# Performance work log

Measured on AMD Instinct MI355X. Metric: run time of the kernel, lower is better.

The kernel has to match this reference:

```python
import jax, jax.numpy as jnp
import numpy as np

EPS = 1e-8
LN_EPS = 1e-5
DIM, NHEADS = 512, 8
HEAD_DIM = DIM // NHEADS
SCALE = HEAD_DIM ** -0.5
ROLE_VOCAB = 8


def _layernorm(x, g, b):
    mu = x.mean(-1, keepdims=True)
    var = ((x - mu) ** 2).mean(-1, keepdims=True)
    return (x - mu) * jax.lax.rsqrt(var + LN_EPS) * g + b


def setup_inputs() -> dict:
    key = jax.random.key(0)
    ks = jax.random.split(key, 16)
    B, K, L, D = 8, 4, 1024, DIM
    s = 1.0 / np.sqrt(D)
    return {
        "state_repr": jax.random.normal(ks[0], (B, K, L, D), jnp.float32),
        "residue_mask": jax.random.randint(ks[1], (B, K, L), 0, 2) > 0,
        "state_weights": jax.random.uniform(ks[2], (B, K), jnp.float32),
        "state_roles": jax.random.randint(ks[3], (B, K), 0, ROLE_VOCAB),
        "state_present_mask": jnp.ones((B, K), dtype=bool),
        "role_emb": jax.random.normal(ks[4], (ROLE_VOCAB, D), jnp.float32),
        "Wq": jax.random.normal(ks[5], (D, D), jnp.float32) * s,
        "Wk": jax.random.normal(ks[6], (D, D), jnp.float32) * s,
        "Wv": jax.random.normal(ks[7], (D, D), jnp.float32) * s,
        "Wo": jax.random.normal(ks[8], (D, D), jnp.float32) * s,
        "ln1_g": jnp.ones((3 * D,), jnp.float32),
        "ln1_b": jnp.zeros((3 * D,), jnp.float32),
        "Wg1": jax.random.normal(ks[9], (D, 3 * D), jnp.float32) / np.sqrt(3 * D),
        "bg1": jnp.zeros((D,), jnp.float32),
        "Wg2": jax.random.normal(ks[10], (D, D), jnp.float32) * s,
        "bg2": jnp.zeros((D,), jnp.float32),
        "norm_g": jnp.ones((D,), jnp.float32),
        "norm_b": jnp.zeros((D,), jnp.float32),
    }


def _forward(state_repr, residue_mask, state_weights, state_roles, state_present_mask,
             role_emb, Wq, Wk, Wv, Wo, ln1_g, ln1_b, Wg1, bg1, Wg2, bg2, norm_g, norm_b):
    B, K, L, D = state_repr.shape
    H, hd = NHEADS, HEAD_DIM
    roles = jnp.maximum(state_roles, 0)
    role_e = role_emb[roles][:, :, None, :]                       # [B,K,1,D]
    valid = residue_mask & state_present_mask[:, :, None]          # [B,K,L]

    # normalized state weights
    pres = state_present_mask.astype(jnp.float32)
    w = state_weights.astype(jnp.float32) * pres
    denom = w.sum(1, keepdims=True)
    fallback = pres / jnp.maximum(pres.sum(1, keepdims=True), 1.0)
    nsw = jnp.where(denom > EPS, w / jnp.maximum(denom, EPS), fallback)  # [B,K]

    x = (state_repr + role_e) * valid[..., None]
    x = x.transpose(0, 2, 1, 3)                                    # [B,L,K,D]
    valid_rlk = valid.transpose(0, 2, 1)                           # [B,L,K]

    def proj(W):  # torch Linear: y = x @ W.T
        return (x @ W.T).reshape(B, L, K, H, hd).transpose(0, 1, 3, 2, 4)  # [B,L,H,K,hd]

    q, k, v = proj(Wq), proj(Wk), proj(Wv)
    logits = jnp.einsum('blhqd,blhkd->blhqk', q, k) * SCALE
    logits = logits + jnp.log(jnp.maximum(nsw, EPS))[:, None, None, None, :]
    key_mask = valid_rlk[:, :, None, None, :]                      # [B,L,1,1,K]
    logits = jnp.where(key_mask, logits, -jnp.inf)
    attn = jax.nn.softmax(logits, axis=-1)
    attn = jnp.nan_to_num(attn, nan=0.0, posinf=0.0, neginf=0.0)
    attn_out = jnp.einsum('blhqk,blhkd->blhqd', attn, v)
    attn_out = attn_out.transpose(0, 1, 3, 2, 4).reshape(B, L, K, D)
    attn_out = (attn_out @ Wo.T) * valid_rlk[..., None]

    swr = nsw[:, None, :] * valid_rlk.astype(jnp.float32)          # [B,L,K]
    swr = swr / jnp.maximum(swr.sum(-1, keepdims=True), EPS)
    weighted_mean = jnp.sum(x * swr[..., None], axis=2)            # [B,L,D]
    attn_pooled = jnp.sum(attn_out * swr[..., None], axis=2)

    max_in = jnp.where(valid_rlk[..., None], x, -1e9)
    max_feat = max_in.max(axis=2)
    has_any = valid_rlk.any(axis=2, keepdims=True)
    max_feat = jnp.where(has_any, max_feat, 0.0)

    fusion_base = 0.5 * (attn_pooled + weighted_mean)
    gate_in = jnp.concatenate([attn_pooled, weighted_mean, max_feat], axis=-1)
    h = _layernorm(gate_in, ln1_g, ln1_b)
    h = jax.nn.gelu(h @ Wg1.T + bg1, approximate=False)
    gate = jax.nn.sigmoid(h @ Wg2.T + bg2)
    fused = gate * fusion_base + (1.0 - gate) * max_feat
    fused = _layernorm(fused + weighted_mean, norm_g, norm_b)

    attn_mean = attn.mean(axis=(2, 3))                             # [B,L,K]
    return fused, attn_pooled, weighted_mean, max_feat, attn_mean, nsw


def reference(state_repr, residue_mask, state_weights, state_roles, state_present_mask,
              role_emb, Wq, Wk, Wv, Wo, ln1_g, ln1_b, Wg1, bg1, Wg2, bg2, norm_g, norm_b):
    return _forward(state_repr, residue_mask, state_weights, state_roles, state_present_mask,
                    role_emb, Wq, Wk, Wv, Wo, ln1_g, ln1_b, Wg1, bg1, Wg2, bg2, norm_g, norm_b)
```

## Files before the change

kernel.cpp:

```cpp
#include <hip/hip_runtime.h>
#include <math.h>

#define BB 8
#define KK 4
#define LL 1024
#define DD 512
#define HD 64
#define D3 1536
#define MM (BB*LL*KK)
#define BL (BB*LL)
#define SCALE 0.125f
#define EPSF 1e-8f
#define LN_EPSF 1e-5f

typedef _Float16 hfrag __attribute__((ext_vector_type(8)));
typedef float f32x4 __attribute__((ext_vector_type(4)));

__device__ __forceinline__ unsigned short f2h(float f) {
    _Float16 h = (_Float16)f;
    unsigned short u; __builtin_memcpy(&u, &h, 2); return u;
}
__device__ __forceinline__ float h2f(unsigned short u) {
    _Float16 h; __builtin_memcpy(&h, &u, 2); return (float)h;
}

__device__ __forceinline__ void glds16(const unsigned short* g, unsigned short* l) {
    __builtin_amdgcn_global_load_lds(
        (const __attribute__((address_space(1))) void*)g,
        (__attribute__((address_space(3))) void*)l, 16, 0, 0);
}

__device__ __forceinline__ void nsw_compute(const float* sw, const int* pres,
                                            int b, float* nswv) {
    float w[KK], pr[KK]; float denom = 0.f, ps = 0.f;
    #pragma unroll
    for (int k = 0; k < KK; ++k) {
        pr[k] = pres[b*KK + k] ? 1.f : 0.f;
        w[k]  = sw[b*KK + k] * pr[k];
        denom += w[k]; ps += pr[k];
    }
    #pragma unroll
    for (int k = 0; k < KK; ++k)
        nswv[k] = (denom > EPSF) ? w[k] / fmaxf(denom, EPSF)
                                 : pr[k] / fmaxf(ps, 1.f);
}

#define WSZ 262144
#define OG1 1048576
#define OG2 1835008
#define WTOT 2097152
__global__ __launch_bounds__(256) void cvt_weights(
        const float* __restrict__ Wq, const float* __restrict__ Wk,
        const float* __restrict__ Wv, const float* __restrict__ Wo,
        const float* __restrict__ Wg1, const float* __restrict__ Wg2,
        unsigned short* __restrict__ dst) {
    int t = blockIdx.x * 256 + threadIdx.x;
    int e = t * 4;
    const float* src; int off;
    if      (e < WSZ)    { src = Wq;  off = e; }
    else if (e < 2*WSZ)  { src = Wk;  off = e - WSZ; }
    else if (e < 3*WSZ)  { src = Wv;  off = e - 2*WSZ; }
    else if (e < OG1)    { src = Wo;  off = e - 3*WSZ; }
    else if (e < OG2)    { src = Wg1; off = e - OG1; }
    else                 { src = Wg2; off = e - OG2; }
    float4 v = *(const float4*)(src + off);
    ushort4 o;
    o.x = f2h(v.x); o.y = f2h(v.y); o.z = f2h(v.z); o.w = f2h(v.w);
    *(ushort4*)(dst + e) = o;
}

__global__ __launch_bounds__(256) void buildx_kernel(
        const float* __restrict__ SR, const int* __restrict__ residue,
        const int* __restrict__ pres, const int* __restrict__ roles,
        const float* __restrict__ role_emb, const float* __restrict__ sw,
        unsigned short* __restrict__ Xh, float* __restrict__ rowmask,
        float* __restrict__ out_wm, float* __restrict__ out_mx,
        float* __restrict__ f_nsw) {
    int t  = blockIdx.x * 256 + threadIdx.x;
    int bl = t >> 7;
    int d4 = (t & 127) << 2;
    int b  = bl >> 10, l = bl & 1023;
    float nswv[KK];
    nsw_compute(sw, pres, b, nswv);
    float mk[KK], swr[KK];
    float ssum = 0.f, many = 0.f;
    #pragma unroll
    for (int k = 0; k < KK; ++k) {
        int bk = b*KK + k;
        bool valid = (residue[(size_t)bk*LL + l] != 0) && (pres[bk] != 0);
        mk[k]  = valid ? 1.f : 0.f;
        swr[k] = nswv[k] * mk[k];
        ssum += swr[k]; many += mk[k];
    }
    float inv = 1.f / fmaxf(ssum, EPSF);
    bool hasany = many > 0.5f;
    float wmx = 0.f, wmy = 0.f, wmz = 0.f, wmw = 0.f;
    float mxx = -1e9f, mxy = -1e9f, mxz = -1e9f, mxw = -1e9f;
    #pragma unroll
    for (int k = 0; k < KK; ++k) {
        int bk = b*KK + k;
        int role = roles[bk]; if (role < 0) role = 0;
        float4 sr = *(const float4*)(SR + ((size_t)bk*LL + l)*DD + d4);
        float4 re = *(const float4*)(role_emb + (size_t)role*DD + d4);
        float xx = (sr.x + re.x)*mk[k], xy = (sr.y + re.y)*mk[k];
        float xz = (sr.z + re.z)*mk[k], xw = (sr.w + re.w)*mk[k];
        ushort4 xs; xs.x = f2h(xx); xs.y = f2h(xy); xs.z = f2h(xz); xs.w = f2h(xw);
        *(ushort4*)(Xh + (size_t)(bl*KK + k)*DD + d4) = xs;
        float s = swr[k]*inv;
        wmx = fmaf(xx, s, wmx); wmy = fmaf(xy, s, wmy);
        wmz = fmaf(xz, s, wmz); wmw = fmaf(xw, s, wmw);
        if (mk[k] > 0.5f) {
            mxx = fmaxf(mxx, xx); mxy = fmaxf(mxy, xy);
            mxz = fmaxf(mxz, xz); mxw = fmaxf(mxw, xw);
        }
    }
    if (!hasany) { mxx = mxy = mxz = mxw = 0.f; }
    float4 wmv; wmv.x = wmx; wmv.y = wmy; wmv.z = wmz; wmv.w = wmw;
    float4 mxv; mxv.x = mxx; mxv.y = mxy; mxv.z = mxz; mxv.w = mxw;
    *(float4*)(out_wm + (size_t)bl*DD + d4) = wmv;
    *(float4*)(out_mx + (size_t)bl*DD + d4) = mxv;
    if (d4 == 0) {
        #pragma unroll
        for (int k = 0; k < KK; ++k) rowmask[bl*KK + k] = mk[k];
    }
    if (blockIdx.x == 0 && threadIdx.x < BB*KK) {
        int bb = threadIdx.x >> 2, kk2 = threadIdx.x & 3;
        float nv[KK];
        nsw_compute(sw, pres, bb, nv);
        f_nsw[threadIdx.x] = nv[kk2];
    }
}

template<int TM, int EPI, int OUTH, int QKVR, int SWZ>
__global__ __launch_bounds__(256) void gemm_mfma(
        const unsigned short* __restrict__ A, const unsigned short* __restrict__ W,
        void* __restrict__ Cv, int M, int N, int Kd,
        const float* __restrict__ bias, const float* __restrict__ rowmask) {
    constexpr int FI = TM / 32;
    __shared__ __align__(16) unsigned short As[TM*32];
    __shared__ __align__(16) unsigned short Bs[128*32];
    const int tid  = threadIdx.x;
    const int wave = tid >> 6, lane = tid & 63;
    int m0, n0;
    if (SWZ) {
        int id = blockIdx.x;
        int c = id & 7, j = id >> 3;
        int mloc = j / 12;
        m0 = (c*32 + mloc) * TM;
        n0 = (j - mloc*12) * 128;
    } else {
        m0 = blockIdx.y * TM; n0 = blockIdx.x * 128;
    }
    const int srow = lane >> 2;
    const int scol = (lane & 3) << 3;
    const int arow = (TM == 128) ? (wave*32 + srow)
                   : (TM == 64)  ? (wave*16 + srow)
                   :               ((wave & 1)*16 + srow);
    const bool astage = (TM >= 64) || (wave < 2);
    const unsigned short* Ag0 = A + (size_t)(m0 + arow) * Kd + scol;
    const unsigned short* Ag1 = Ag0 + (size_t)16 * Kd;
    unsigned short* Al0 = As + arow*32 + scol;
    unsigned short* Al1 = Al0 + 16*32;
    const unsigned short* Wp0 = W + (size_t)(n0 + wave*32 + srow) * Kd + scol;
    const unsigned short* Wp1 = Wp0 + (size_t)16 * Kd;
    unsigned short* Bl0 = Bs + (wave*32 + srow)*32 + scol;
    unsigned short* Bl1 = Bl0 + 16*32;
    const int wr = (wave >> 1) * (TM/2);
    const int wc = (wave & 1) * 64;
    const int fr = lane & 15;
    const int fq = (lane >> 4) * 8;
    f32x4 acc[FI][4] = {};
    for (int k0 = 0; k0 < Kd; k0 += 32) {
        if (astage)    glds16(Ag0 + k0, Al0);
        if (TM == 128) glds16(Ag1 + k0, Al1);
        glds16(Wp0 + k0, Bl0);
        glds16(Wp1 + k0, Bl1);
        __syncthreads();
        hfrag af[FI], bf[4];
        #pragma unroll
        for (int i = 0; i < FI; ++i)
            af[i] = *(const hfrag*)(As + (wr + i*16 + fr)*32 + fq);
        #pragma unroll
        for (int j = 0; j < 4; ++j)
            bf[j] = *(const hfrag*)(Bs + (wc + j*16 + fr)*32 + fq);
        #pragma unroll
        for (int i = 0; i < FI; ++i)
            #pragma unroll
            for (int j = 0; j < 4; ++j)
                acc[i][j] = __builtin_amdgcn_mfma_f32_16x16x32_f16(af[i], bf[j], acc[i][j], 0, 0, 0);
        __syncthreads();
    }
    unsigned short* Ch = (unsigned short*)Cv;
    int Nout = N, colbase = n0;
    if (QKVR) {
        const int seg = n0 >> 9;
        Ch = (unsigned short*)Cv + (size_t)seg * M * 512;
        Nout = 512;
        colbase = n0 - (seg << 9);
    }
    #pragma unroll
    for (int i = 0; i < FI; ++i) {
        const int row = m0 + wr + i*16 + (lane >> 4)*4;
        #pragma unroll
        for (int j = 0; j < 4; ++j) {
            const int col = colbase + wc + j*16 + (lane & 15);
            float bv = (EPI == 2) ? bias[col] : 0.f;
            #pragma unroll
            for (int r = 0; r < 4; ++r) {
                float v = acc[i][j][r];
                if (EPI == 2) { v += bv; v = 0.5f * v * (1.f + erff(v * 0.70710678118654752f)); }
                if (OUTH) Ch[(size_t)(row + r) * Nout + col] = f2h(v);
                else      ((float*)Cv)[(size_t)(row + r) * Nout + col] = v;
            }
        }
    }
}

__global__ __launch_bounds__(256) void wo_pool_kernel(
        const unsigned short* __restrict__ A,
        const unsigned short* __restrict__ W,
        const float* __restrict__ sw, const int* __restrict__ pres,
        const float* __restrict__ rmask,
        const float* __restrict__ in_wm, const float* __restrict__ in_mx,
        const float* __restrict__ ln1_g, const float* __restrict__ ln1_b,
        float* __restrict__ out_ap, unsigned short* __restrict__ hin) {
    __shared__ __align__(16) unsigned short As[32*32];
    __shared__ __align__(16) unsigned short Bs[512*32];
    const int tid = threadIdx.x, wave = tid >> 6, lane = tid & 63;
    const int m0 = blockIdx.x * 32;
    const int srow = lane >> 2, scol = (lane & 3) << 3;
    const unsigned short* Ag = A + (size_t)(m0 + wave*16 + srow)*512 + scol;
    unsigned short* Al = As + (wave*16 + srow)*32 + scol;
    const int brow = wave*128 + srow;
    const unsigned short* Wg = W + (size_t)brow*512 + scol;
    unsigned short* Blb = Bs + brow*32 + scol;
    const int q = lane >> 4, frl = lane & 15;
    const int fq = q * 8;
    f32x4 acc[2][8] = {};
    for (int k0 = 0; k0 < 512; k0 += 32) {
        if (wave < 2) glds16(Ag + k0, Al);
        #pragma unroll
        for (int i = 0; i < 8; ++i)
            glds16(Wg + (size_t)i*16*512 + k0, Blb + i*16*32);
        __syncthreads();
        hfrag af[2], bf[8];
        #pragma unroll
        for (int i = 0; i < 2; ++i)
            af[i] = *(const hfrag*)(As + (i*16 + frl)*32 + fq);
        #pragma unroll
        for (int j = 0; j < 8; ++j)
            bf[j] = *(const hfrag*)(Bs + (wave*128 + j*16 + frl)*32 + fq);
        #pragma unroll
        for (int i = 0; i < 2; ++i)
            #pragma unroll
            for (int j = 0; j < 8; ++j)
                acc[i][j] = __builtin_amdgcn_mfma_f32_16x16x32_f16(af[i], bf[j], acc[i][j], 0, 0, 0);
        __syncthreads();
    }
    float* ap_s = (float*)Bs;
    const int bl0 = m0 >> 2;
    const int b = bl0 >> 10;
    float nv[KK];
    nsw_compute(sw, pres, b, nv);
    #pragma unroll
    for (int i = 0; i < 2; ++i) {
        int bl_loc = i*4 + q;
        int blg = bl0 + bl_loc;
        float s4[KK]; float ssum = 0.f;
        #pragma unroll
        for (int k = 0; k < KK; ++k) { s4[k] = nv[k] * rmask[blg*4 + k]; ssum += s4[k]; }
        float inv = 1.f / fmaxf(ssum, EPSF);
        #pragma unroll
        for (int j = 0; j < 8; ++j) {
            float ap = 0.f;
            #pragma unroll
            for (int r = 0; r < KK; ++r) ap = fmaf(s4[r]*inv, acc[i][j][r], ap);
            ap_s[bl_loc*512 + wave*128 + j*16 + frl] = ap;
        }
    }
    __syncthreads();
    const int blq = tid >> 5;
    const int c0  = (tid & 31) * 16;
    const int blg = bl0 + blq;
    float4 ap4[4], wm4[4], mx4[4];
    #pragma unroll
    for (int v = 0; v < 4; ++v) {
        ap4[v] = *(const float4*)(ap_s + blq*512 + c0 + v*4);
        wm4[v] = *(const float4*)(in_wm + (size_t)blg*512 + c0 + v*4);
        mx4[v] = *(const float4*)(in_mx + (size_t)blg*512 + c0 + v*4);
    }
    float s = 0.f, s2 = 0.f;
    #pragma unroll
    for (int c = 0; c < 16; ++c) {
        float ap = ((const float*)ap4)[c];
        float wm = ((const float*)wm4)[c];
        float mx = ((const float*)mx4)[c];
        s += ap + wm + mx; s2 += ap*ap + wm*wm + mx*mx;
    }
    #pragma unroll
    for (int o = 1; o < 32; o <<= 1) {
        s  += __shfl_xor(s,  o, 32);
        s2 += __shfl_xor(s2, o, 32);
    }
    float mu = s * (1.f/(float)D3);
    float var = s2 * (1.f/(float)D3) - mu*mu;
    float rstd = rsqrtf(var + LN_EPSF);
    #pragma unroll
    for (int v = 0; v < 4; ++v)
        *(float4*)(out_ap + (size_t)blg*512 + c0 + v*4) = ap4[v];
    #pragma unroll
    for (int seg = 0; seg < 3; ++seg) {
        const float* src = (seg == 0) ? (const float*)ap4
                         : (seg == 1) ? (const float*)wm4 : (const float*)mx4;
        int gofs = seg*512 + c0;
        #pragma unroll
        for (int v = 0; v < 4; ++v) {
            float4 g4 = *(const float4*)(ln1_g + gofs + v*4);
            float4 b4 = *(const float4*)(ln1_b + gofs + v*4);
            ushort4 o;
            o.x = f2h((src[v*4+0]-mu)*rstd*g4.x + b4.x);
            o.y = f2h((src[v*4+1]-mu)*rstd*g4.y + b4.y);
            o.z = f2h((src[v*4+2]-mu)*rstd*g4.z + b4.z);
            o.w = f2h((src[v*4+3]-mu)*rstd*g4.w + b4.w);
            *(ushort4*)(hin + (size_t)blg*D3 + gofs + v*4) = o;
        }
    }
}

__global__ __launch_bounds__(256) void wg2_final_kernel(
        const unsigned short* __restrict__ A,
        const unsigned short* __restrict__ W,
        const float* __restrict__ bg2,
        const float* __restrict__ in_ap, const float* __restrict__ in_wm,
        const float* __restrict__ in_mx,
        const float* __restrict__ norm_g, const float* __restrict__ norm_b,
        float* __restrict__ fused) {
    __shared__ __align__(16) unsigned short As[16*32];
    __shared__ __align__(16) unsigned short Bs[512*32];
    __shared__ float rs[16*4], rq[16*4];
    const int tid = threadIdx.x, wave = tid >> 6, lane = tid & 63;
    const int m0 = blockIdx.x * 16;
    const int srow = lane >> 2, scol = (lane & 3) << 3;
    const unsigned short* Ag = A + (size_t)(m0 + srow)*512 + scol;
    unsigned short* Al = As + srow*32 + scol;
    const int brow = wave*128 + srow;
    const unsigned short* Wg = W + (size_t)brow*512 + scol;
    unsigned short* Blb = Bs + brow*32 + scol;
    const int q = lane >> 4, frl = lane & 15;
    const int fq = q * 8;
    f32x4 acc[8] = {};
    for (int k0 = 0; k0 < 512; k0 += 32) {
        if (wave == 0) glds16(Ag + k0, Al);
        #pragma unroll
        for (int i = 0; i < 8; ++i)
            glds16(Wg + (size_t)i*16*512 + k0, Blb + i*16*32);
        __syncthreads();
        hfrag af, bf[8];
        af = *(const hfrag*)(As + frl*32 + fq);
        #pragma unroll
        for (int j = 0; j < 8; ++j)
            bf[j] = *(const hfrag*)(Bs + (wave*128 + j*16 + frl)*32 + fq);
        #pragma unroll
        for (int j = 0; j < 8; ++j)
            acc[j] = __builtin_amdgcn_mfma_f32_16x16x32_f16(af, bf[j], acc[j], 0, 0, 0);
        __syncthreads();
    }
    float pre[8][4];
    float s[4] = {}, s2[4] = {};
    #pragma unroll
    for (int j = 0; j < 8; ++j) {
        int col = wave*128 + j*16 + frl;
        float bv = bg2[col];
        #pragma unroll
        for (int r = 0; r < 4; ++r) {
            int row = m0 + q*4 + r;
            float g = 1.f / (1.f + expf(-(acc[j][r] + bv)));
            float ap = in_ap[(size_t)row*512 + col];
            float wm = in_wm[(size_t)row*512 + col];
            float mx = in_mx[(size_t)row*512 + col];
            float p = g*0.5f*(ap + wm) + (1.f - g)*mx + wm;
            pre[j][r] = p;
            s[r] += p; s2[r] += p*p;
        }
    }
    #pragma unroll
    for (int r = 0; r < 4; ++r) {
        #pragma unroll
        for (int o = 1; o < 16; o <<= 1) {
            s[r]  += __shfl_xor(s[r],  o, 64);
            s2[r] += __shfl_xor(s2[r], o, 64);
        }
        if (frl == 0) {
            rs[(q*4+r)*4 + wave] = s[r];
            rq[(q*4+r)*4 + wave] = s2[r];
        }
    }
    __syncthreads();
    float mu[4], rstd[4];
    #pragma unroll
    for (int r = 0; r < 4; ++r) {
        int rl = q*4 + r;
        float ts  = rs[rl*4] + rs[rl*4+1] + rs[rl*4+2] + rs[rl*4+3];
        float tq  = rq[rl*4] + rq[rl*4+1] + rq[rl*4+2] + rq[rl*4+3];
        float m = ts * (1.f/(float)DD);
        float v = tq * (1.f/(float)DD) - m*m;
        mu[r] = m; rstd[r] = rsqrtf(v + LN_EPSF);
    }
    #pragma unroll
    for (int j = 0; j < 8; ++j) {
        int col = wave*128 + j*16 + frl;
        float g = norm_g[col], bb = norm_b[col];
        #pragma unroll
        for (int r = 0; r < 4; ++r) {
            int row = m0 + q*4 + r;
            fused[(size_t)row*512 + col] = (pre[j][r]-mu[r])*rstd[r]*g + bb;
        }
    }
}

__global__ __launch_bounds__(256) void attn_kernel(
        unsigned short* Qb ,
        const unsigned short* __restrict__ Kb, const unsigned short* __restrict__ Vb,
        const float* __restrict__ sw, const int* __restrict__ pres,
        const float* __restrict__ rowmask,
        float* __restrict__ attn_mean_out) {
    __shared__ float qs[KK][DD];
    __shared__ float ksm[KK][DD];
    __shared__ float vs[KK][DD];
    __shared__ float att[128];
    __shared__ float lw[KK], mk[KK];
    int bl = blockIdx.x, b = bl >> 10, mb = bl * KK;
    int tid = threadIdx.x;
    const ushort4* q4 = (const ushort4*)(Qb + (size_t)mb*DD);
    const ushort4* k4 = (const ushort4*)(Kb + (size_t)mb*DD);
    const ushort4* v4 = (const ushort4*)(Vb + (size_t)mb*DD);
    #pragma unroll
    for (int p = 0; p < 2; ++p) {
        int idx = p*256 + tid;
        int k = idx >> 7, dd = (idx & 127) << 2;
        ushort4 a = q4[idx];
        qs[k][dd] = h2f(a.x); qs[k][dd+1] = h2f(a.y); qs[k][dd+2] = h2f(a.z); qs[k][dd+3] = h2f(a.w);
        ushort4 c = k4[idx];
        ksm[k][dd] = h2f(c.x); ksm[k][dd+1] = h2f(c.y); ksm[k][dd+2] = h2f(c.z); ksm[k][dd+3] = h2f(c.w);
        ushort4 e = v4[idx];
        vs[k][dd] = h2f(e.x); vs[k][dd+1] = h2f(e.y); vs[k][dd+2] = h2f(e.z); vs[k][dd+3] = h2f(e.w);
    }
    if (tid < KK) {
        float nv[KK];
        nsw_compute(sw, pres, b, nv);
        lw[tid] = logf(fmaxf(nv[tid], EPSF));
        mk[tid] = rowmask[mb + tid];
    }
    __syncthreads();
    if (tid < 128) {
        int h = tid >> 4, i = (tid >> 2) & 3, j = tid & 3;
        float s = 0.f;
        #pragma unroll 16
        for (int d = 0; d < HD; ++d) s = fmaf(qs[i][h*HD + d], ksm[j][h*HD + d], s);
        float lg = s * SCALE + lw[j];
        att[tid] = (mk[j] > 0.5f) ? lg : -INFINITY;
    }
    __syncthreads();
    if (tid < 32) {
        int base = tid * 4;
        float l0 = att[base], l1 = att[base+1], l2 = att[base+2], l3 = att[base+3];
        float m = fmaxf(fmaxf(l0, l1), fmaxf(l2, l3));
        if (m == -INFINITY) {
            att[base] = att[base+1] = att[base+2] = att[base+3] = 0.f;
        } else {
            float e0 = expf(l0 - m), e1 = expf(l1 - m), e2 = expf(l2 - m), e3 = expf(l3 - m);
            float inv = 1.f / (e0 + e1 + e2 + e3);
            att[base] = e0*inv; att[base+1] = e1*inv; att[base+2] = e2*inv; att[base+3] = e3*inv;
        }
    }
    __syncthreads();
    if (tid < KK) {
        float s = 0.f;
        for (int hi = 0; hi < 32; ++hi) s += att[hi*4 + tid];
        attn_mean_out[(size_t)bl*KK + tid] = s * (1.f/32.f);
    }
    float outv[8];
    #pragma unroll
    for (int p = 0; p < 8; ++p) {
        int idx = p*256 + tid;
        int i = idx >> 9, dc = idx & 511, h = dc >> 6;
        float s = 0.f;
        #pragma unroll
        for (int j = 0; j < KK; ++j) s = fmaf(att[h*16 + i*4 + j], vs[j][dc], s);
        outv[p] = s;
    }
    #pragma unroll
    for (int p = 0; p < 8; ++p) {
        int idx = p*256 + tid;
        int i = idx >> 9, dc = idx & 511;
        Qb[(size_t)(mb+i)*DD + dc] = f2h(outv[p]);
    }
}

extern "C" void kernel_launch(void* const* d_in, const int* in_sizes, int n_in,
                              void* d_out, int out_size, void* d_ws, size_t ws_size,
                              hipStream_t stream) {
    const float* SR      = (const float*)d_in[0];
    const int*   residue = (const int*)d_in[1];
    const float* sw      = (const float*)d_in[2];
    const int*   roles   = (const int*)d_in[3];
    const int*   pres    = (const int*)d_in[4];
    const float* role_emb= (const float*)d_in[5];
    const float* Wq      = (const float*)d_in[6];
    const float* Wk      = (const float*)d_in[7];
    const float* Wv      = (const float*)d_in[8];
    const float* Wo      = (const float*)d_in[9];
    const float* ln1_g   = (const float*)d_in[10];
    const float* ln1_b   = (const float*)d_in[11];
    const float* Wg1     = (const float*)d_in[12];
    const float* bg1     = (const float*)d_in[13];
    const float* Wg2     = (const float*)d_in[14];
    const float* bg2     = (const float*)d_in[15];
    const float* norm_g  = (const float*)d_in[16];
    const float* norm_b  = (const float*)d_in[17];

    float* out = (float*)d_out;
    const size_t BLD = (size_t)BL * DD;
    float* f_fused = out;
    float* f_ap    = out + BLD;
    float* f_wm    = out + 2*BLD;
    float* f_mx    = out + 3*BLD;
    float* f_am    = out + 4*BLD;
    float* f_nsw   = out + 4*BLD + (size_t)BL*KK;

    char* base = (char*)d_ws;
    const size_t MD2 = (size_t)MM * DD * 2;
    unsigned short* Xh = (unsigned short*)(base);
    unsigned short* Qh = (unsigned short*)(base + MD2);
    unsigned short* Kh = (unsigned short*)(base + 2*MD2);
    unsigned short* Vh = (unsigned short*)(base + 3*MD2);
    unsigned short* Wb = (unsigned short*)(base + 4*MD2);
    float* rmask = (float*)(base + 4*MD2 + (size_t)WTOT*2);
    unsigned short* AOh  = Qh;
    unsigned short* Hin  = Vh;
    unsigned short* Hbuf = Xh;
    const unsigned short* Wqkv = Wb;
    const unsigned short* Woh  = Wb + 3*WSZ;
    const unsigned short* Wg1h = Wb + OG1;
    const unsigned short* Wg2h = Wb + OG2;

    dim3 blk(256);

    cvt_weights<<<WTOT/1024, blk, 0, stream>>>(Wq, Wk, Wv, Wo, Wg1, Wg2, Wb);
    buildx_kernel<<<(BL*128)/256, blk, 0, stream>>>(SR, residue, pres, roles, role_emb,
                                                    sw, Xh, rmask, f_wm, f_mx, f_nsw);

    gemm_mfma<128,0,1,1,1><<<dim3(3072), blk, 0, stream>>>(
        Xh, Wqkv, Qh, MM, 1536, DD, nullptr, nullptr);

    attn_kernel<<<BL, blk, 0, stream>>>(Qh, Kh, Vh, sw, pres, rmask, f_am);

    wo_pool_kernel<<<dim3(MM/32), blk, 0, stream>>>(
        AOh, Woh, sw, pres, rmask, f_wm, f_mx, ln1_g, ln1_b, f_ap, Hin);

    gemm_mfma<32,2,1,0,0><<<dim3(4, BL/32), blk, 0, stream>>>(
        Hin, Wg1h, Hbuf, BL, DD, D3, bg1, nullptr);

    wg2_final_kernel<<<dim3(BL/16), blk, 0, stream>>>(
        Hbuf, Wg2h, bg2, f_ap, f_wm, f_mx, norm_g, norm_b, f_fused);
}
```

Before: 386.4 us.

## Replace QKV GEMM with 256x256-tile 8-wave kernel using 4-stage LDS pipeline

Adds a dedicated QKV projection kernel that uses 512-thread blocks computing 256x256 output tiles. It stages A and B tiles into a 4-deep LDS ring buffer with direct global-to-LDS loads and an XOR swizzle, waits on explicit vmcnt values, and raises MFMA priority. Blocks are remapped so tiles are spread across XCDs. The aim is more data reuse per tile and overlap of loads with MFMA work on the largest GEMM. In exchange it uses 128 KB of LDS per block and hand-tuned barriers, which limits occupancy and is fragile.

```diff
diff --git a/kernel.cpp b/kernel.cpp
--- a/kernel.cpp
+++ b/kernel.cpp
@@ -216,6 +216,124 @@
     }
 }
 
+__global__ __launch_bounds__(512, 2) void gemm_qkv_8p(
+        const unsigned short* __restrict__ A, const unsigned short* __restrict__ W,
+        unsigned short* __restrict__ Cbase) {
+    __shared__ __align__(16) unsigned short smem[65536];
+    const int tid  = threadIdx.x;
+    const int wave = tid >> 6, lane = tid & 63;
+    const int id = blockIdx.x;
+    const int wg = (id & 7) * 96 + (id >> 3);
+    const int m0 = (wg / 6) * 256;
+    const int n0 = (wg % 6) * 256;
+    const int wm = wave >> 2, wn = wave & 3;
+    const int fr = lane & 15, q = lane >> 4;
+    const int c0 = (wave << 6) | lane;
+    const int r0 = c0 >> 2, cc0 = c0 & 3;
+    const int c1 = c0 + 512;
+    const int r1 = c1 >> 2, cc1 = c1 & 3;
+    const unsigned short* Ag0 = A + (size_t)(m0 + r0)*512 + ((cc0 ^ ((r0 >> 1) & 3)) << 3);
+    const unsigned short* Ag1 = A + (size_t)(m0 + r1)*512 + ((cc1 ^ ((r1 >> 1) & 3)) << 3);
+    const unsigned short* Wp0 = W + (size_t)(n0 + r0)*512 + ((cc0 ^ ((r0 >> 1) & 3)) << 3);
+    const unsigned short* Wp1 = W + (size_t)(n0 + r1)*512 + ((cc1 ^ ((r1 >> 1) & 3)) << 3);
+    const int lA0 = c0 << 3, lA1 = c1 << 3;
+    int aoff[8], boff[4];
+    #pragma unroll
+    for (int mf = 0; mf < 8; ++mf) {
+        int row = (wm << 7) + (mf << 4) + fr;
+        aoff[mf] = (row << 5) + ((q ^ ((row >> 1) & 3)) << 3);
+    }
+    #pragma unroll
+    for (int nf = 0; nf < 4; ++nf) {
+        int row = (wn << 6) + (nf << 4) + fr;
+        boff[nf] = (row << 5) + ((q ^ ((row >> 1) & 3)) << 3);
+    }
+    f32x4 acc[8][4] = {};
+
+#define VMWAIT(N) asm volatile("s_waitcnt vmcnt(" #N ")" ::: "memory")
+#define LGKM0()   asm volatile("s_waitcnt lgkmcnt(0)" ::: "memory")
+#define STAGE_A(tt) do { unsigned short* _d = smem + (((tt) & 3) << 14); \
+        const int _ko = (tt) << 5; \
+        glds16(Ag0 + _ko, _d + lA0); glds16(Ag1 + _ko, _d + lA1); } while (0)
+#define STAGE_B(tt) do { unsigned short* _d = smem + ((((tt) & 3) << 14) + 8192); \
+        const int _ko = (tt) << 5; \
+        glds16(Wp0 + _ko, _d + lA0); glds16(Wp1 + _ko, _d + lA1); } while (0)
+#define MFROW(ai, areg) \
+        acc[ai][0] = __builtin_amdgcn_mfma_f32_16x16x32_f16(areg, b0, acc[ai][0], 0, 0, 0); \
+        acc[ai][1] = __builtin_amdgcn_mfma_f32_16x16x32_f16(areg, b1, acc[ai][1], 0, 0, 0); \
+        acc[ai][2] = __builtin_amdgcn_mfma_f32_16x16x32_f16(areg, b2, acc[ai][2], 0, 0, 0); \
+        acc[ai][3] = __builtin_amdgcn_mfma_f32_16x16x32_f16(areg, b3, acc[ai][3], 0, 0, 0);
+#define TILE(t, STG, VM) do { \
+        const unsigned short* _Ab = smem + (((t) & 3) << 14); \
+        const unsigned short* _Bb = _Ab + 8192; \
+        VMWAIT(VM); \
+        __builtin_amdgcn_s_barrier(); \
+        __builtin_amdgcn_sched_barrier(0); \
+        hfrag b0 = *(const hfrag*)(_Bb + boff[0]); \
+        hfrag b1 = *(const hfrag*)(_Bb + boff[1]); \
+        hfrag b2 = *(const hfrag*)(_Bb + boff[2]); \
+        hfrag b3 = *(const hfrag*)(_Bb + boff[3]); \
+        { \
+            hfrag a0_ = *(const hfrag*)(_Ab + aoff[0]); \
+            hfrag a1_ = *(const hfrag*)(_Ab + aoff[1]); \
+            hfrag a2_ = *(const hfrag*)(_Ab + aoff[2]); \
+            hfrag a3_ = *(const hfrag*)(_Ab + aoff[3]); \
+            if (STG) STAGE_A((t) + 3); \
+            __builtin_amdgcn_s_barrier(); \
+            LGKM0(); \
+            __builtin_amdgcn_sched_barrier(0); \
+            __builtin_amdgcn_s_setprio(1); \
+            MFROW(0, a0_) MFROW(1, a1_) MFROW(2, a2_) MFROW(3, a3_) \
+            __builtin_amdgcn_s_setprio(0); \
+            __builtin_amdgcn_s_barrier(); \
+        } \
+        { \
+            hfrag a4_ = *(const hfrag*)(_Ab + aoff[4]); \
+            hfrag a5_ = *(const hfrag*)(_Ab + aoff[5]); \
+            hfrag a6_ = *(const hfrag*)(_Ab + aoff[6]); \
+            hfrag a7_ = *(const hfrag*)(_Ab + aoff[7]); \
+            if (STG) STAGE_B((t) + 3); \
+            __builtin_amdgcn_s_barrier(); \
+            LGKM0(); \
+            __builtin_amdgcn_sched_barrier(0); \
+            __builtin_amdgcn_s_setprio(1); \
+            MFROW(4, a4_) MFROW(5, a5_) MFROW(6, a6_) MFROW(7, a7_) \
+            __builtin_amdgcn_s_setprio(0); \
+            __builtin_amdgcn_s_barrier(); \
+        } \
+    } while (0)
+
+    STAGE_A(0); STAGE_B(0);
+    STAGE_A(1); STAGE_B(1);
+    STAGE_A(2); STAGE_B(2);
+    for (int t = 0; t < 13; ++t) TILE(t, 1, 8);
+    TILE(13, 0, 8);
+    TILE(14, 0, 4);
+    TILE(15, 0, 0);
+#undef TILE
+#undef MFROW
+#undef STAGE_A
+#undef STAGE_B
+#undef VMWAIT
+#undef LGKM0
+
+    const int gc0 = n0 + (wn << 6);
+    const int seg = gc0 >> 9;
+    unsigned short* Cs = Cbase + (size_t)seg * ((size_t)MM * 512);
+    const int cb = gc0 & 511;
+    #pragma unroll
+    for (int mf = 0; mf < 8; ++mf) {
+        const int grow = m0 + (wm << 7) + (mf << 4) + (q << 2);
+        #pragma unroll
+        for (int nf = 0; nf < 4; ++nf) {
+            const int col = cb + (nf << 4) + fr;
+            #pragma unroll
+            for (int r = 0; r < 4; ++r)
+                Cs[(size_t)(grow + r) * 512 + col] = f2h(acc[mf][nf][r]);
+        }
+    }
+}
+
 __global__ __launch_bounds__(256) void wo_pool_kernel(
         const unsigned short* __restrict__ A,
         const unsigned short* __restrict__ W,
@@ -550,8 +668,7 @@
     buildx_kernel<<<(BL*128)/256, blk, 0, stream>>>(SR, residue, pres, roles, role_emb,
                                                     sw, Xh, rmask, f_wm, f_mx, f_nsw);
 
-    gemm_mfma<128,0,1,1,1><<<dim3(3072), blk, 0, stream>>>(
-        Xh, Wqkv, Qh, MM, 1536, DD, nullptr, nullptr);
+    gemm_qkv_8p<<<dim3(768), dim3(512), 0, stream>>>(Xh, Wqkv, Qh);
 
     attn_kernel<<<BL, blk, 0, stream>>>(Qh, Kh, Vh, sw, pres, rmask, f_am);
 
```

Measured after the change: 381.0 us. About the same (-1.4%).

## Replace QKV GEMM with register-only MFMA kernel using double-buffered global loads

Applied to the files above, without the earlier changes.

Adds a dedicated QKV projection kernel that loads A and W fragments straight from global memory into registers, double-buffered two K-steps ahead, with no LDS staging or barriers. It also remaps block IDs so consecutive blocks are spread across the output tile grid, and raises wave priority around the MFMA bursts. This targets LDS traffic and synchronization overhead in the old shared-memory tiled GEMM. In exchange, data is no longer shared between waves through LDS, so the same global data is read more times and relies on L2 for reuse, and the 64-wide fragment arrays raise register pressure.

```diff
diff --git a/kernel.cpp b/kernel.cpp
--- a/kernel.cpp
+++ b/kernel.cpp
@@ -216,6 +216,66 @@
     }
 }
 
+__global__ __launch_bounds__(256, 3) void gemm_qkv_reg(
+        const unsigned short* __restrict__ A, const unsigned short* __restrict__ W,
+        unsigned short* __restrict__ Cbase) {
+    const int tid  = threadIdx.x;
+    const int wave = tid >> 6, lane = tid & 63;
+    const int id = blockIdx.x;
+    const int wg = (id & 7) * 384 + (id >> 3);
+    const int m0 = (wg / 12) * 128;
+    const int n0 = (wg % 12) * 128;
+    const int wm = wave >> 1, wn = wave & 1;
+    const int fr = lane & 15, q = lane >> 4;
+    int aoff[4], boff[4];
+    #pragma unroll
+    for (int i = 0; i < 4; ++i) {
+        aoff[i] = (m0 + wm*64 + i*16 + fr) * 512 + q*8;
+        boff[i] = (n0 + wn*64 + i*16 + fr) * 512 + q*8;
+    }
+    hfrag a[2][4], b[2][4];
+    f32x4 acc[4][4] = {};
+
+#define LDGEN(g, k0) do { \
+        _Pragma("unroll") \
+        for (int i = 0; i < 4; ++i) { \
+            a[g][i] = *(const hfrag*)(A + aoff[i] + (k0)); \
+            b[g][i] = *(const hfrag*)(W + boff[i] + (k0)); \
+        } } while (0)
+
+    LDGEN(0, 0);
+    LDGEN(1, 32);
+    #pragma unroll
+    for (int t = 0; t < 16; ++t) {
+        const int g = t & 1;
+        __builtin_amdgcn_s_setprio(1);
+        #pragma unroll
+        for (int i = 0; i < 4; ++i)
+            #pragma unroll
+            for (int j = 0; j < 4; ++j)
+                acc[i][j] = __builtin_amdgcn_mfma_f32_16x16x32_f16(a[g][i], b[g][j], acc[i][j], 0, 0, 0);
+        __builtin_amdgcn_s_setprio(0);
+        if (t < 14) LDGEN(g, (t + 2) * 32);
+    }
+#undef LDGEN
+
+    const int gc0 = n0 + (wn << 6);
+    const int seg = gc0 >> 9;
+    unsigned short* Cs = Cbase + (size_t)seg * ((size_t)MM * 512);
+    const int cb = gc0 & 511;
+    #pragma unroll
+    for (int mf = 0; mf < 4; ++mf) {
+        const int grow = m0 + (wm << 6) + (mf << 4) + (q << 2);
+        #pragma unroll
+        for (int nf = 0; nf < 4; ++nf) {
+            const int col = cb + (nf << 4) + fr;
+            #pragma unroll
+            for (int r = 0; r < 4; ++r)
+                Cs[(size_t)(grow + r) * 512 + col] = f2h(acc[mf][nf][r]);
+        }
+    }
+}
+
 __global__ __launch_bounds__(256) void wo_pool_kernel(
         const unsigned short* __restrict__ A,
         const unsigned short* __restrict__ W,
@@ -550,8 +610,7 @@
     buildx_kernel<<<(BL*128)/256, blk, 0, stream>>>(SR, residue, pres, roles, role_emb,
                                                     sw, Xh, rmask, f_wm, f_mx, f_nsw);
 
-    gemm_mfma<128,0,1,1,1><<<dim3(3072), blk, 0, stream>>>(
-        Xh, Wqkv, Qh, MM, 1536, DD, nullptr, nullptr);
+    gemm_qkv_reg<<<dim3(3072), blk, 0, stream>>>(Xh, Wqkv, Qh);
 
     attn_kernel<<<BL, blk, 0, stream>>>(Qh, Kh, Vh, sw, pres, rmask, f_am);
 
```

Result: slower. 497.6 us (+28.8%).
